# Optimization experiments

Hardware: AMD Instinct MI355X
Metric: run time of the kernel (lower is better)

The kernel has to match this reference:

```python
import jax, jax.numpy as jnp
import numpy as np

K_STEPS = 10
ALPHA = 0.9
N_NODES = 16384
N_CLASSES = 64
N_EDGES = 524288


def setup_inputs() -> dict:
    key = jax.random.key(0)
    k1, k2, k3 = jax.random.split(key, 3)
    masked_y_true = jax.random.normal(k1, (N_NODES, N_CLASSES), dtype=jnp.float32)
    K = jax.random.normal(k2, (N_NODES, N_NODES), dtype=jnp.float32)
    edge_index = jax.random.randint(k3, (2, N_EDGES), 0, N_NODES, dtype=jnp.int32)
    return {"masked_y_true": masked_y_true, "K": K, "edge_index": edge_index}


def reference(masked_y_true, K, edge_index):
    src, dst = edge_index[0], edge_index[1]
    # DAD normalization: w_e = deg(src)^-1/2 * deg(dst)^-1/2
    deg = jnp.zeros((N_NODES,), jnp.float32).at[dst].add(1.0)
    dinv = jax.lax.rsqrt(jnp.maximum(deg, 1.0))
    w = dinv[src] * dinv[dst]  # [E]

    def spmm(x):
        # A @ x with A in edge-list form (static sparsity, reused each step)
        return jax.ops.segment_sum(w[:, None] * x[src], dst, num_segments=N_NODES)

    def prop_step(_, y):
        return ALPHA * spmm(y) + (1.0 - ALPHA) * y

    y = jax.lax.fori_loop(0, K_STEPS, prop_step, masked_y_true)
    y = K @ y
    y = jax.lax.fori_loop(0, K_STEPS, prop_step, y)
    return y
```

## Files before the change

kernel.cpp:

```cpp
#include <hip/hip_runtime.h>

#define NN 16384
#define NC 64
#define NE 524288
#define ALPHA 0.9f
#define KSTEPS 10

typedef _Float16 f16;
typedef _Float16 f16x4 __attribute__((ext_vector_type(4)));
typedef _Float16 f16x8 __attribute__((ext_vector_type(8)));
typedef float f32x4 __attribute__((ext_vector_type(4)));
typedef int i32x16 __attribute__((ext_vector_type(16)));

#define MEMB   asm volatile("" ::: "memory")
#define SCHED0 __builtin_amdgcn_sched_barrier(0)

__global__ __launch_bounds__(256) void deg_kernel(const int* __restrict__ dst,
                                                  unsigned* __restrict__ deg) {
    int e = blockIdx.x * 256 + threadIdx.x;
    atomicAdd(&deg[dst[e]], 1u);
}

__global__ __launch_bounds__(1024) void scan_kernel(const unsigned* __restrict__ deg,
                                                    float* __restrict__ dinv,
                                                    unsigned* __restrict__ rowoff,
                                                    unsigned* __restrict__ cursor) {
    __shared__ unsigned part[1024];
    const int t = threadIdx.x;
    const int base = t * 16;
    unsigned local[16];
    unsigned s = 0;
    #pragma unroll
    for (int i = 0; i < 16; ++i) {
        local[i] = s;
        s += (deg[base + i] + 15u) & ~15u;
    }
    part[t] = s;
    __syncthreads();
    for (int off = 1; off < 1024; off <<= 1) {
        unsigned v = (t >= off) ? part[t - off] : 0u;
        __syncthreads();
        part[t] += v;
        __syncthreads();
    }
    const unsigned ex = (t == 0) ? 0u : part[t - 1];
    #pragma unroll
    for (int i = 0; i < 16; ++i) {
        unsigned ro = ex + local[i];
        rowoff[base + i] = ro;
        cursor[base + i] = ro;
        unsigned d = deg[base + i];
        dinv[base + i] = rsqrtf(fmaxf((float)d, 1.0f));
    }
    if (t == 1023) rowoff[NN] = part[1023];
}

__global__ __launch_bounds__(256) void fill_kernel(const int* __restrict__ src,
                                                   const int* __restrict__ dst,
                                                   const float* __restrict__ dinv,
                                                   unsigned* __restrict__ cursor,
                                                   int2* __restrict__ csr) {
    int e = blockIdx.x * 256 + threadIdx.x;
    int s = src[e], d = dst[e];
    float w = dinv[s] * dinv[d];
    unsigned p = atomicAdd(&cursor[d], 1u);
    csr[p] = make_int2(s, __float_as_int(w));
}

__global__ __launch_bounds__(256) void prop_kernel(const float* __restrict__ x,
                                                   float* __restrict__ y,
                                                   const unsigned* __restrict__ rowoff,
                                                   const int* __restrict__ csr) {
    const int lane = threadIdx.x & 63;
    const int n = __builtin_amdgcn_readfirstlane(blockIdx.x * 4 + (threadIdx.x >> 6));
    const unsigned beg = rowoff[n];
    const unsigned np = (rowoff[n + 1] - beg) >> 4;
    float acc0 = 0.f, acc1 = 0.f;
    if (np) {
        i32x16 e0 = *(const i32x16*)(csr + 2 * beg);
        i32x16 e1 = *(const i32x16*)(csr + 2 * beg + 16);
        float xv0[8], xv1[8];
        #pragma unroll
        for (int j = 0; j < 8; ++j) xv0[j] = x[(unsigned)e0[2 * j] * 64u + lane];
        #pragma unroll
        for (int j = 0; j < 8; ++j) xv1[j] = x[(unsigned)e1[2 * j] * 64u + lane];
        for (unsigned p = 1; p < np; ++p) {
            const i32x16 f0 = *(const i32x16*)(csr + 2 * (beg + p * 16));
            const i32x16 f1 = *(const i32x16*)(csr + 2 * (beg + p * 16) + 16);
            #pragma unroll
            for (int j = 0; j < 8; ++j) {
                const float w = __int_as_float(e0[2 * j + 1]);
                if (j & 1) acc1 = fmaf(w, xv0[j], acc1);
                else       acc0 = fmaf(w, xv0[j], acc0);
            }
            #pragma unroll
            for (int j = 0; j < 8; ++j) xv0[j] = x[(unsigned)f0[2 * j] * 64u + lane];
            #pragma unroll
            for (int j = 0; j < 8; ++j) {
                const float w = __int_as_float(e1[2 * j + 1]);
                if (j & 1) acc1 = fmaf(w, xv1[j], acc1);
                else       acc0 = fmaf(w, xv1[j], acc0);
            }
            #pragma unroll
            for (int j = 0; j < 8; ++j) xv1[j] = x[(unsigned)f1[2 * j] * 64u + lane];
            e0 = f0; e1 = f1;
        }
        #pragma unroll
        for (int j = 0; j < 8; ++j) {
            const float w = __int_as_float(e0[2 * j + 1]);
            if (j & 1) acc1 = fmaf(w, xv0[j], acc1);
            else       acc0 = fmaf(w, xv0[j], acc0);
        }
        #pragma unroll
        for (int j = 0; j < 8; ++j) {
            const float w = __int_as_float(e1[2 * j + 1]);
            if (j & 1) acc1 = fmaf(w, xv1[j], acc1);
            else       acc0 = fmaf(w, xv1[j], acc0);
        }
    }
    y[n * 64 + lane] = ALPHA * (acc0 + acc1) + (1.0f - ALPHA) * x[n * 64 + lane];
}

__global__ __launch_bounds__(256) void ysplit_kernel(const float* __restrict__ y,
                                                     f16* __restrict__ yhT,
                                                     f16* __restrict__ ylT) {
    __shared__ f16 hb[64][72];
    __shared__ f16 lb[64][72];
    const int t = threadIdx.x;
    const int b = blockIdx.x;
    const int kl = t >> 2;
    const int cq = (t & 3) * 16;
    #pragma unroll
    for (int i = 0; i < 4; ++i) {
        float4 v = *(const float4*)&y[(size_t)(b * 64 + kl) * 64 + cq + i * 4];
        float vv[4] = {v.x, v.y, v.z, v.w};
        #pragma unroll
        for (int j = 0; j < 4; ++j) {
            int c = cq + i * 4 + j;
            f16 h = (f16)vv[j];
            float r = vv[j] - (float)h;
            hb[c][kl] = h;
            lb[c][kl] = (f16)r;
        }
    }
    __syncthreads();
    const int c = t >> 2;
    const int kq = (t & 3) * 16;
    #pragma unroll
    for (int s2 = 0; s2 < 2; ++s2) {
        int slot = (kq >> 3) + s2;
        int dslot = slot ^ (c & 7);
        f16x8 hv, lv;
        #pragma unroll
        for (int j = 0; j < 8; ++j) { hv[j] = hb[c][kq + s2 * 8 + j]; lv[j] = lb[c][kq + s2 * 8 + j]; }
        *(f16x8*)&yhT[(size_t)c * NN + b * 64 + dslot * 8] = hv;
        *(f16x8*)&ylT[(size_t)c * NN + b * 64 + dslot * 8] = lv;
    }
}

__device__ inline void gload16(const void* g, void* l) {
    __builtin_amdgcn_global_load_lds((const __attribute__((address_space(1))) void*)g,
                                     (__attribute__((address_space(3))) void*)l, 16, 0, 0);
}

#define AH_OFF 0
#define AL_OFF 16384
#define YP_OFF 32768

__global__ __launch_bounds__(256, 2) void gemm_kernel(const float* __restrict__ A,
                                                      const f16* __restrict__ yhT,
                                                      const f16* __restrict__ ylT,
                                                      float* __restrict__ z) {
    __shared__ char lds[65536];
    const int t = threadIdx.x;
    const int w = t >> 6;
    const int l = t & 63;
    const size_t row0 = (size_t)blockIdx.x * 128;
    const int kbase = blockIdx.y * 2048;

    f32x4 acc[2][4];
    #pragma unroll
    for (int m = 0; m < 2; ++m)
        #pragma unroll
        for (int n = 0; n < 4; ++n)
            acc[m][n] = (f32x4){0.f, 0.f, 0.f, 0.f};

    const int arow_l = w * 4 + (l >> 4);
    const int acol = (l & 15) * 4;
    const int ycr = l >> 3;
    const int yco = (l & 7) * 8;

    float4 aA[8], aB[8];

    auto loadA = [&](float4 (&dst)[8], int tile) {
        const int kt = kbase + tile * 64;
        #pragma unroll
        for (int i = 0; i < 8; ++i)
            dst[i] = *(const float4*)&A[(row0 + i * 16 + arow_l) * 16384 + kt + acol];
    };
    auto issueY = [&](int tile, int cur) {
        const int kt = kbase + tile * 64;
        #pragma unroll
        for (int j = 0; j < 2; ++j) {
            const int i = 2 * w + j;
            gload16(yhT + (size_t)(i * 8 + ycr) * NN + kt + yco,
                    lds + YP_OFF + cur * 16384 + i * 1024);
            gload16(ylT + (size_t)(i * 8 + ycr) * NN + kt + yco,
                    lds + YP_OFF + cur * 16384 + 8192 + i * 1024);
        }
    };
    auto writeA = [&](const float4 (&src)[8]) {
        #pragma unroll
        for (int i = 0; i < 8; ++i) {
            const int r = i * 16 + arow_l;
            float v[4] = {src[i].x, src[i].y, src[i].z, src[i].w};
            f16x4 h4, l4;
            #pragma unroll
            for (int j = 0; j < 4; ++j) {
                f16 h = (f16)v[j];
                h4[j] = h;
                l4[j] = (f16)(v[j] - (float)h);
            }
            const int byte = r * 128 + (((((l & 15) >> 1)) ^ (r & 7)) << 4) + (l & 1) * 8;
            *(f16x4*)(lds + AH_OFF + byte) = h4;
            *(f16x4*)(lds + AL_OFF + byte) = l4;
        }
    };
    auto mfmaTile = [&](int cur) {
        #pragma unroll
        for (int s = 0; s < 2; ++s) {
            const int slot = s * 4 + (l >> 4);
            f16x8 ah[2], alo[2];
            #pragma unroll
            for (int m = 0; m < 2; ++m) {
                const int r = w * 32 + m * 16 + (l & 15);
                const int byte = r * 128 + ((slot ^ (r & 7)) << 4);
                ah[m]  = *(const f16x8*)(lds + AH_OFF + byte);
                alo[m] = *(const f16x8*)(lds + AL_OFF + byte);
            }
            #pragma unroll
            for (int n = 0; n < 4; ++n) {
                const int c = n * 16 + (l & 15);
                const int byte = c * 128 + ((slot ^ (c & 7)) << 4);
                const f16x8 bh = *(const f16x8*)(lds + YP_OFF + cur * 16384 + byte);
                const f16x8 bl = *(const f16x8*)(lds + YP_OFF + cur * 16384 + 8192 + byte);
                #pragma unroll
                for (int m = 0; m < 2; ++m) {
                    acc[m][n] = __builtin_amdgcn_mfma_f32_16x16x32_f16(ah[m],  bh, acc[m][n], 0, 0, 0);
                    acc[m][n] = __builtin_amdgcn_mfma_f32_16x16x32_f16(ah[m],  bl, acc[m][n], 0, 0, 0);
                    acc[m][n] = __builtin_amdgcn_mfma_f32_16x16x32_f16(alo[m], bh, acc[m][n], 0, 0, 0);
                }
            }
        }
    };

    loadA(aA, 0); MEMB;
    issueY(0, 0); MEMB;
    loadA(aB, 1); MEMB;
    writeA(aA);
    asm volatile("s_waitcnt vmcnt(8)" ::: "memory");  SCHED0;
    asm volatile("s_waitcnt lgkmcnt(0)" ::: "memory"); SCHED0;
    __builtin_amdgcn_s_barrier(); SCHED0;

#define GEMM_ITER(TILE, CUR, SETF, SETW)                                      \
    issueY((TILE) + 1, (CUR) ^ 1); MEMB;                                      \
    loadA(SETF, (TILE) + 2); MEMB;                                            \
    mfmaTile(CUR);                                                            \
    MEMB; SCHED0;                                                             \
    __builtin_amdgcn_s_barrier();                 \
    writeA(SETW);                                  \
    asm volatile("s_waitcnt vmcnt(8)" ::: "memory");  SCHED0;   \
    asm volatile("s_waitcnt lgkmcnt(0)" ::: "memory"); SCHED0;                \
    __builtin_amdgcn_s_barrier(); SCHED0;

    for (int tp = 0; tp < 15; ++tp) {
        const int t0 = 2 * tp;
        GEMM_ITER(t0,     0, aA, aB);
        GEMM_ITER(t0 + 1, 1, aB, aA);
    }
    issueY(31, 1); MEMB;
    mfmaTile(0);
    MEMB; SCHED0;
    __builtin_amdgcn_s_barrier();
    writeA(aB);
    asm volatile("s_waitcnt vmcnt(0)" ::: "memory");  SCHED0;
    asm volatile("s_waitcnt lgkmcnt(0)" ::: "memory"); SCHED0;
    __builtin_amdgcn_s_barrier(); SCHED0;
    mfmaTile(1);
#undef GEMM_ITER

    #pragma unroll
    for (int m = 0; m < 2; ++m)
        #pragma unroll
        for (int n = 0; n < 4; ++n)
            #pragma unroll
            for (int q = 0; q < 4; ++q) {
                const size_t gr = row0 + w * 32 + m * 16 + (l >> 4) * 4 + q;
                const int gc = n * 16 + (l & 15);
                atomicAdd(&z[gr * 64 + gc], acc[m][n][q]);
            }
}

extern "C" void kernel_launch(void* const* d_in, const int* in_sizes, int n_in,
                              void* d_out, int out_size, void* d_ws, size_t ws_size,
                              hipStream_t stream) {
    const float* ytrue = (const float*)d_in[0];
    const float* Kmat  = (const float*)d_in[1];
    const int*   eidx  = (const int*)d_in[2];
    const int* esrc = eidx;
    const int* edst = eidx + NE;
    float* out = (float*)d_out;

    char* ws = (char*)d_ws;
    size_t off = 0;
    auto alloc = [&](size_t bytes) -> void* {
        void* p = ws + off;
        off += (bytes + 255) & ~(size_t)255;
        return p;
    };
    const size_t CSR_ENTRIES = (size_t)NE + 16 * NN;
    unsigned* deg    = (unsigned*)alloc((size_t)NN * 4);
    unsigned* rowoff = (unsigned*)alloc((size_t)(NN + 1) * 4);
    unsigned* cursor = (unsigned*)alloc((size_t)NN * 4);
    float*    dinv   = (float*)alloc((size_t)NN * 4);
    int2*     csr    = (int2*)alloc(CSR_ENTRIES * 8);
    float*    yA     = (float*)alloc((size_t)NN * NC * 4);
    float*    yB     = (float*)alloc((size_t)NN * NC * 4);
    f16*      yhT    = (f16*)alloc((size_t)NC * NN * 2);
    f16*      ylT    = (f16*)alloc((size_t)NC * NN * 2);

    hipMemsetAsync(deg, 0, (size_t)NN * 4, stream);
    hipMemsetAsync(csr, 0, CSR_ENTRIES * 8, stream);
    deg_kernel<<<NE / 256, 256, 0, stream>>>(edst, deg);
    scan_kernel<<<1, 1024, 0, stream>>>(deg, dinv, rowoff, cursor);
    fill_kernel<<<NE / 256, 256, 0, stream>>>(esrc, edst, dinv, cursor, csr);

    const float* cur = ytrue;
    float* bufs[2] = {yA, yB};
    int pb = 0;
    for (int s = 0; s < KSTEPS; ++s) {
        float* nxt = bufs[pb];
        pb ^= 1;
        prop_kernel<<<NN / 4, 256, 0, stream>>>(cur, nxt, rowoff, (const int*)csr);
        cur = nxt;
    }

    ysplit_kernel<<<NN / 64, 256, 0, stream>>>(cur, yhT, ylT);

    float* z = (cur == yA) ? yB : yA;
    hipMemsetAsync(z, 0, (size_t)NN * NC * 4, stream);
    gemm_kernel<<<dim3(128, 8), 256, 0, stream>>>(Kmat, yhT, ylT, z);

    float* other = (z == yA) ? yB : yA;
    const float* c2 = z;
    for (int s = 0; s < KSTEPS; ++s) {
        float* nxt = (s == KSTEPS - 1) ? out : other;
        prop_kernel<<<NN / 4, 256, 0, stream>>>(c2, nxt, rowoff, (const int*)csr);
        other = (float*)c2;
        c2 = nxt;
    }
}
```

Measured before the change: 529.6 us.

## Deepen GEMM prefetch pipeline to three stages for A registers and Y LDS

Extends the GEMM main loop from double to triple buffering: Y tiles are now prefetched two tiles ahead into three LDS buffers and A tiles three tiles ahead into three register sets, with the wait count relaxed accordingly. The aim is to hide more global-memory latency behind the MFMA work. In exchange, LDS per block grows to 80 KB and register use rises with a third float4[8] set, which may cut occupancy below the two blocks per CU requested by the launch bounds. Tail iterations clamp to tile 31 and issue redundant loads rather than having a separate epilogue.

```diff
diff --git a/kernel.cpp b/kernel.cpp
--- a/kernel.cpp
+++ b/kernel.cpp
@@ -171,7 +171,7 @@
                                                       const f16* __restrict__ yhT,
                                                       const f16* __restrict__ ylT,
                                                       float* __restrict__ z) {
-    __shared__ char lds[65536];
+    __shared__ char lds[81920];
     const int t = threadIdx.x;
     const int w = t >> 6;
     const int l = t & 63;
@@ -190,7 +190,7 @@
     const int ycr = l >> 3;
     const int yco = (l & 7) * 8;
 
-    float4 aA[8], aB[8];
+    float4 a0[8], a1[8], a2[8];
 
     auto loadA = [&](float4 (&dst)[8], int tile) {
         const int kt = kbase + tile * 64;
@@ -198,15 +198,15 @@
         for (int i = 0; i < 8; ++i)
             dst[i] = *(const float4*)&A[(row0 + i * 16 + arow_l) * 16384 + kt + acol];
     };
-    auto issueY = [&](int tile, int cur) {
+    auto issueY = [&](int tile, int buf) {
         const int kt = kbase + tile * 64;
         #pragma unroll
         for (int j = 0; j < 2; ++j) {
             const int i = 2 * w + j;
             gload16(yhT + (size_t)(i * 8 + ycr) * NN + kt + yco,
-                    lds + YP_OFF + cur * 16384 + i * 1024);
+                    lds + YP_OFF + buf * 16384 + i * 1024);
             gload16(ylT + (size_t)(i * 8 + ycr) * NN + kt + yco,
-                    lds + YP_OFF + cur * 16384 + 8192 + i * 1024);
+                    lds + YP_OFF + buf * 16384 + 8192 + i * 1024);
         }
     };
     auto writeA = [&](const float4 (&src)[8]) {
@@ -226,7 +226,7 @@
             *(f16x4*)(lds + AL_OFF + byte) = l4;
         }
     };
-    auto mfmaTile = [&](int cur) {
+    auto mfmaTile = [&](int buf) {
         #pragma unroll
         for (int s = 0; s < 2; ++s) {
             const int slot = s * 4 + (l >> 4);
@@ -242,8 +242,8 @@
             for (int n = 0; n < 4; ++n) {
                 const int c = n * 16 + (l & 15);
                 const int byte = c * 128 + ((slot ^ (c & 7)) << 4);
-                const f16x8 bh = *(const f16x8*)(lds + YP_OFF + cur * 16384 + byte);
-                const f16x8 bl = *(const f16x8*)(lds + YP_OFF + cur * 16384 + 8192 + byte);
+                const f16x8 bh = *(const f16x8*)(lds + YP_OFF + buf * 16384 + byte);
+                const f16x8 bl = *(const f16x8*)(lds + YP_OFF + buf * 16384 + 8192 + byte);
                 #pragma unroll
                 for (int m = 0; m < 2; ++m) {
                     acc[m][n] = __builtin_amdgcn_mfma_f32_16x16x32_f16(ah[m],  bh, acc[m][n], 0, 0, 0);
@@ -254,39 +254,35 @@
         }
     };
 
-    loadA(aA, 0); MEMB;
+    loadA(a0, 0); MEMB;
     issueY(0, 0); MEMB;
-    loadA(aB, 1); MEMB;
-    writeA(aA);
-    asm volatile("s_waitcnt vmcnt(8)" ::: "memory");  SCHED0;
+    loadA(a1, 1); MEMB;
+    issueY(1, 1); MEMB;
+    loadA(a2, 2); MEMB;
+    writeA(a0);
+    asm volatile("s_waitcnt vmcnt(20)" ::: "memory"); SCHED0;
     asm volatile("s_waitcnt lgkmcnt(0)" ::: "memory"); SCHED0;
     __builtin_amdgcn_s_barrier(); SCHED0;
 
-#define GEMM_ITER(TILE, CUR, SETF, SETW)                                      \
-    issueY((TILE) + 1, (CUR) ^ 1); MEMB;                                      \
-    loadA(SETF, (TILE) + 2); MEMB;                                            \
-    mfmaTile(CUR);                                                            \
+#define GEMM_ITER(TILE, BUFC, BUFY, SETF, SETW)                               \
+    issueY(((TILE) + 2 < 32) ? (TILE) + 2 : 31, BUFY); MEMB;                  \
+    loadA(SETF, ((TILE) + 3 < 32) ? (TILE) + 3 : 31); MEMB;                   \
+    mfmaTile(BUFC);                                                           \
     MEMB; SCHED0;                                                             \
-    __builtin_amdgcn_s_barrier();                 \
-    writeA(SETW);                                  \
-    asm volatile("s_waitcnt vmcnt(8)" ::: "memory");  SCHED0;   \
+    __builtin_amdgcn_s_barrier();               \
+    writeA(SETW);                                     \
+    asm volatile("s_waitcnt vmcnt(20)" ::: "memory");  SCHED0;    \
     asm volatile("s_waitcnt lgkmcnt(0)" ::: "memory"); SCHED0;                \
     __builtin_amdgcn_s_barrier(); SCHED0;
 
-    for (int tp = 0; tp < 15; ++tp) {
-        const int t0 = 2 * tp;
-        GEMM_ITER(t0,     0, aA, aB);
-        GEMM_ITER(t0 + 1, 1, aB, aA);
-    }
-    issueY(31, 1); MEMB;
-    mfmaTile(0);
-    MEMB; SCHED0;
-    __builtin_amdgcn_s_barrier();
-    writeA(aB);
-    asm volatile("s_waitcnt vmcnt(0)" ::: "memory");  SCHED0;
-    asm volatile("s_waitcnt lgkmcnt(0)" ::: "memory"); SCHED0;
-    __builtin_amdgcn_s_barrier(); SCHED0;
-    mfmaTile(1);
+    for (int tt = 0; tt < 10; ++tt) {
+        const int t0 = 3 * tt;
+        GEMM_ITER(t0,     0, 2, a0, a1);
+        GEMM_ITER(t0 + 1, 1, 0, a1, a2);
+        GEMM_ITER(t0 + 2, 2, 1, a2, a0);
+    }
+    GEMM_ITER(30, 0, 2, a0, a1);
+    GEMM_ITER(31, 1, 0, a1, a2);
 #undef GEMM_ITER
 
     #pragma unroll
```

New measurement: 542.0 us. 1.02x slower.
